# Kernel tuning notes

Measured on AMD Instinct MI355X. Metric: run time of the kernel, lower is better.

Reference implementation:

```python
import jax, jax.numpy as jnp
import numpy as np

OBS, HOR, PD, HID, NH, PROTO = 8, 8, 128, 256, 8, 32
B, N = 8, 4096

def _gelu(x):
    return jax.nn.gelu(x, approximate=False)  # torch nn.GELU default is exact erf

def setup_inputs():
    key = jax.random.key(0)
    ks = iter(jax.random.split(key, 40))
    nrm = lambda shape, s=0.02: jax.random.normal(next(ks), shape, dtype=jnp.float32) * s
    return {
        'obs_points': jax.random.normal(next(ks), (B, N, OBS, 2), dtype=jnp.float32),
        'obs_vis': jax.random.randint(next(ks), (B, N, OBS), 0, 2).astype(bool),
        'rel_xy': jax.random.normal(next(ks), (B, N, 2), dtype=jnp.float32),
        'anchor_obs': jax.random.normal(next(ks), (B, OBS, 2), dtype=jnp.float32),
        'anchor_obs_vel': jax.random.normal(next(ks), (B, OBS, 2), dtype=jnp.float32),
        'semantic_feat': jax.random.normal(next(ks), (B, N, 10), dtype=jnp.float32),
        'ln_w': jnp.ones((OBS * 7,), jnp.float32),
        'ln_b': jnp.zeros((OBS * 7,), jnp.float32),
        'enc_w1': nrm((OBS * 7, PD)), 'enc_b1': jnp.zeros((PD,), jnp.float32),
        'enc_w2': nrm((PD, PD)), 'enc_b2': jnp.zeros((PD,), jnp.float32),
        'time_embed': nrm((HOR, HID)),
        'anchor_w': nrm((OBS * 4, HID)), 'anchor_b': jnp.zeros((HID,), jnp.float32),
        'query_w': nrm((PD, HID)), 'query_b': jnp.zeros((HID,), jnp.float32),
        'in_proj_w': nrm((HID, 3 * HID)), 'in_proj_b': jnp.zeros((3 * HID,), jnp.float32),
        'out_proj_w': nrm((HID, HID)), 'out_proj_b': jnp.zeros((HID,), jnp.float32),
        'ah_w': nrm((HID, 2)), 'ah_b': jnp.zeros((2,), jnp.float32),
        'rh_w1': nrm((HID + PD + 2, HID)), 'rh_b1': jnp.zeros((HID,), jnp.float32),
        'rh_w2': nrm((HID, 2)), 'rh_b2': jnp.zeros((2,), jnp.float32),
        'vh_w1': nrm((HID + PD, HID // 2)), 'vh_b1': jnp.zeros((HID // 2,), jnp.float32),
        'vh_w2': nrm((HID // 2, 1)), 'vh_b2': jnp.zeros((1,), jnp.float32),
        'sh_w': nrm((HID, PROTO)), 'sh_b': jnp.zeros((PROTO,), jnp.float32),
    }

def reference(obs_points, obs_vis, rel_xy, anchor_obs, anchor_obs_vel, semantic_feat,
              ln_w, ln_b, enc_w1, enc_b1, enc_w2, enc_b2, time_embed,
              anchor_w, anchor_b, query_w, query_b, in_proj_w, in_proj_b,
              out_proj_w, out_proj_b, ah_w, ah_b, rh_w1, rh_b1, rh_w2, rh_b2,
              vh_w1, vh_b1, vh_w2, vh_b2, sh_w, sh_b):
    del semantic_feat  # unused, matches original
    Bc, Nc, T, _ = obs_points.shape
    # ---- PointTraceEncoder ----
    vel = jnp.concatenate([jnp.zeros_like(obs_points[:, :, :1]),
                           obs_points[:, :, 1:] - obs_points[:, :, :-1]], axis=2)
    rel = jnp.broadcast_to(rel_xy[:, :, None, :], (Bc, Nc, T, 2))
    feat = jnp.concatenate([obs_points, vel, obs_vis.astype(jnp.float32)[..., None], rel],
                           axis=-1).reshape(Bc, Nc, T * 7)
    mu = feat.mean(-1, keepdims=True)
    var = ((feat - mu) ** 2).mean(-1, keepdims=True)
    x = (feat - mu) / jnp.sqrt(var + 1e-5) * ln_w + ln_b
    point_tokens = _gelu(_gelu(x @ enc_w1 + enc_b1) @ enc_w2 + enc_b2)  # [B,N,PD]
    # ---- queries / memory ----
    anchor_feat = jnp.concatenate([anchor_obs, anchor_obs_vel], -1).reshape(Bc, -1)
    tq = time_embed[None] + (anchor_feat @ anchor_w + anchor_b)[:, None]  # [B,HOR,HID]
    mem = point_tokens @ query_w + query_b  # [B,N,HID]
    # ---- multi-head cross attention ----
    D = tq.shape[-1]; dh = D // NH
    q = tq @ in_proj_w[:, :D] + in_proj_b[:D]
    k = mem @ in_proj_w[:, D:2 * D] + in_proj_b[D:2 * D]
    v = mem @ in_proj_w[:, 2 * D:] + in_proj_b[2 * D:]
    qh = q.reshape(Bc, -1, NH, dh).transpose(0, 2, 1, 3)
    kh = k.reshape(Bc, -1, NH, dh).transpose(0, 2, 1, 3)
    vh = v.reshape(Bc, -1, NH, dh).transpose(0, 2, 1, 3)
    attn = jax.nn.softmax(jnp.einsum('bhqd,bhkd->bhqk', qh, kh) / jnp.sqrt(jnp.float32(dh)), axis=-1)
    o = jnp.einsum('bhqk,bhkd->bhqd', attn, vh).transpose(0, 2, 1, 3).reshape(Bc, -1, D)
    future = o @ out_proj_w + out_proj_b  # [B,HOR,HID]
    # ---- heads ----
    last_anchor = anchor_obs[:, -1]
    anchor_delta = 0.1 * jnp.tanh(future @ ah_w + ah_b)
    anchor_pred = last_anchor[:, None] + jnp.cumsum(anchor_delta, axis=1)  # [B,HOR,2]
    Hq = future.shape[1]
    ft_e = jnp.broadcast_to(future[:, :, None, :], (Bc, Hq, Nc, D))
    pt_e = jnp.broadcast_to(point_tokens[:, None], (Bc, Hq, Nc, point_tokens.shape[-1]))
    rel_e = jnp.broadcast_to(rel_xy[:, None], (Bc, Hq, Nc, 2))
    per_point = jnp.concatenate([ft_e, pt_e, rel_e], axis=-1)  # [B,HOR,N,HID+PD+2]
    residual = 0.1 * jnp.tanh(_gelu(per_point @ rh_w1 + rh_b1) @ rh_w2 + rh_b2)
    pred_points = anchor_pred[:, :, None, :] + residual
    vis_logits = (_gelu(per_point[..., :-2] @ vh_w1 + vh_b1) @ vh_w2 + vh_b2)[..., 0]
    sem_logits = future @ sh_w + sh_b
    return (anchor_pred,
            pred_points.transpose(0, 2, 1, 3),   # [B,N,HOR,2]
            vis_logits.transpose(0, 2, 1),       # [B,N,HOR]
            sem_logits)                           # [B,HOR,PROTO]
```

## Files before the change

### kernel.cpp

```cpp
#include <hip/hip_runtime.h>
#include <math.h>

#define BB 8
#define NN 4096
#define TT 8
#define HORQ 8
#define PD 128
#define HID 256
#define NHD 8
#define DH 32
#define FE 56
#define NC2 16
#define CH2 256

typedef __attribute__((ext_vector_type(8))) short short8;
typedef __attribute__((ext_vector_type(4))) float floatx4;
typedef unsigned short ushort_t;

__device__ __forceinline__ float gelu_fast(float x) {
    float x2 = x * x;
    float y2 = x * fmaf(0.0713551f, x2, 1.5957691f);
    float e = __expf(y2);
    return x - x * __builtin_amdgcn_rcpf(1.f + e);
}

__device__ __forceinline__ float tanh_fast(float x) {
    float e = __expf(2.f * x);
    return 1.f - 2.f * __builtin_amdgcn_rcpf(1.f + e);
}

__device__ __forceinline__ ushort_t f2b(float x) {
    union { float f; unsigned u; } c; c.f = x;
    unsigned r = c.u + 0x7fffu + ((c.u >> 16) & 1u);
    return (ushort_t)(r >> 16);
}
__device__ __forceinline__ float b2f(unsigned hi) {
    union { unsigned u; float f; } c; c.u = hi;
    return c.f;
}

__global__ __launch_bounds__(256) void k_fuse(
    const float* __restrict__ qw, const float* __restrict__ qb,
    const float* __restrict__ ipw, const float* __restrict__ ipb,
    float* __restrict__ Wk, float* __restrict__ Wv,
    float* __restrict__ bk, float* __restrict__ bv)
{
    int j = threadIdx.x;
    int blk = blockIdx.x;
    if (blk < PD) {
        float sk = 0.f, sv = 0.f;
        for (int l = 0; l < HID; l++) {
            float w = qw[blk * HID + l];
            sk += w * ipw[l * 768 + 256 + j];
            sv += w * ipw[l * 768 + 512 + j];
        }
        Wk[blk * HID + j] = sk;
        Wv[blk * HID + j] = sv;
    } else {
        float sk = ipb[256 + j], sv = ipb[512 + j];
        for (int l = 0; l < HID; l++) {
            float w = qb[l];
            sk += w * ipw[l * 768 + 256 + j];
            sv += w * ipw[l * 768 + 512 + j];
        }
        bk[j] = sk;
        bv[j] = sv;
    }
}

__global__ __launch_bounds__(256) void k_prep(
    const float* __restrict__ Wk, const float* __restrict__ Wv,
    const float* __restrict__ rw1, const float* __restrict__ vw1,
    const float* __restrict__ w1, const float* __restrict__ w2,
    const float* __restrict__ aobs, const float* __restrict__ avel,
    const float* __restrict__ te, const float* __restrict__ aw, const float* __restrict__ ab,
    const float* __restrict__ ipw, const float* __restrict__ ipb,
    short* __restrict__ Wfrag, short* __restrict__ w1frag, short* __restrict__ w2frag,
    float* __restrict__ qb_)
{
    __shared__ float af[32];
    __shared__ float tqs[HID];
    int tid = threadIdx.x;
    int blk = blockIdx.x;
    int ks = tid >> 6, lane = tid & 63;
    int quad = lane >> 4, c16 = lane & 15;
    if (blk < 56) {
        int nt = blk;
        int n = nt * 16 + c16;
        for (int j = 0; j < 8; j++) {
            int k = ks * 32 + quad * 8 + j;
            float v;
            if (n < 256)      v = Wk[k * HID + n];
            else if (n < 512) v = Wv[k * HID + (n - 256)];
            else if (n < 768) v = rw1[(256 + k) * HID + (n - 512)];
            else              v = vw1[(256 + k) * PD + (n - 768)];
            Wfrag[((nt * 4 + ks) * 64 + lane) * 8 + j] = (short)f2b(v);
        }
    } else if (blk < 64) {
        if (ks < 2) {
            int nt = blk - 56;
            int n = nt * 16 + c16;
            for (int j = 0; j < 8; j++) {
                int k = ks * 32 + quad * 8 + j;
                float v = (k < FE) ? w1[k * PD + n] : 0.f;
                w1frag[((nt * 2 + ks) * 64 + lane) * 8 + j] = (short)f2b(v);
            }
        }
    } else if (blk < 72) {
        int nt = blk - 64;
        int n = nt * 16 + c16;
        for (int j = 0; j < 8; j++) {
            int k = ks * 32 + quad * 8 + j;
            w2frag[((nt * 4 + ks) * 64 + lane) * 8 + j] = (short)f2b(w2[k * PD + n]);
        }
    } else {
        int bh = blk - 72;
        int b = bh >> 3, h = bh & 7;
        if (tid < 32) {
            int t = tid >> 2, m = tid & 3;
            af[tid] = (m < 2) ? aobs[(b * TT + t) * 2 + m] : avel[(b * TT + t) * 2 + (m - 2)];
        }
        __syncthreads();
        float s = te[h * HID + tid] + ab[tid];
        for (int i = 0; i < 32; i++) s += af[i] * aw[i * HID + tid];
        tqs[tid] = s;
        __syncthreads();
        float qv = ipb[tid];
        for (int i = 0; i < HID; i++) qv += tqs[i] * ipw[i * 768 + tid];
        qb_[(size_t)bh * HID + tid] = qv;
    }
}

#define U1_OFF 0
#define XNB_OFF 17408
#define PTB_OFF 26624
#define RXY_OFF 44032
#define MU_OFF 44544
#define RS_OFF 44800
#define SMEM_BYTES 45056

__global__ __launch_bounds__(256) void k_main(
    const float* __restrict__ obs, const int* __restrict__ vis,
    const float* __restrict__ rel,
    const float* __restrict__ lnw, const float* __restrict__ lnb,
    const float* __restrict__ b1, const float* __restrict__ b2,
    const short* __restrict__ Wfrag, const short* __restrict__ w1frag,
    const short* __restrict__ w2frag,
    const float* __restrict__ bk, const float* __restrict__ bv,
    const float* __restrict__ rw1,
    ushort_t* __restrict__ kb, ushort_t* __restrict__ vb,
    ushort_t* __restrict__ P1, ushort_t* __restrict__ P2)
{
    __shared__ __align__(16) char smem[SMEM_BYTES];
    float* xnf = (float*)(smem + U1_OFF);
    short* h1b = (short*)(smem + U1_OFF);
    short* xnb = (short*)(smem + XNB_OFF);
    short* ptb = (short*)(smem + PTB_OFF);
    float* rxyS = (float*)(smem + RXY_OFF);
    float* muS = (float*)(smem + MU_OFF);
    float* rsS = (float*)(smem + RS_OFF);

    int tid = threadIdx.x;
    int w = tid >> 6, lane = tid & 63;
    int quad = lane >> 4, c16 = lane & 15;
    int bn0 = blockIdx.x * 64;

    for (int idx = tid; idx < 64 * FE; idx += 256) {
        int p = idx / FE, e = idx - p * FE;
        int t = e / 7, c = e - t * 7;
        int bn = bn0 + p;
        float v;
        if (c < 2)       v = obs[(bn * TT + t) * 2 + c];
        else if (c < 4)  v = (t == 0) ? 0.f : (obs[(bn * TT + t) * 2 + (c - 2)] - obs[(bn * TT + t - 1) * 2 + (c - 2)]);
        else if (c == 4) v = (float)vis[bn * TT + t];
        else             v = rel[bn * 2 + (c - 5)];
        xnf[p * 57 + e] = v;
    }
    if (tid < 128) rxyS[tid] = rel[bn0 * 2 + tid];
    __syncthreads();

    if (tid < 64) {
        float s = 0.f, ss = 0.f;
        for (int e = 0; e < FE; e++) { float v = xnf[tid * 57 + e]; s += v; ss += v * v; }
        float mu = s * (1.f / FE);
        float var = ss * (1.f / FE) - mu * mu;
        muS[tid] = mu;
        rsS[tid] = rsqrtf(var + 1e-5f);
    }
    __syncthreads();

    for (int idx = tid; idx < 64 * 64; idx += 256) {
        int p = idx >> 6, e = idx & 63;
        float v = 0.f;
        if (e < FE) v = (xnf[p * 57 + e] - muS[p]) * rsS[p] * lnw[e] + lnb[e];
        xnb[p * 72 + e] = (short)f2b(v);
    }
    __syncthreads();

    {
        short8 af1[4][2];
        #pragma unroll
        for (int mt = 0; mt < 4; mt++)
            #pragma unroll
            for (int ks = 0; ks < 2; ks++)
                af1[mt][ks] = *(const short8*)(xnb + (mt * 16 + c16) * 72 + ks * 32 + quad * 8);
        #pragma unroll
        for (int ntl = 0; ntl < 2; ntl++) {
            int nt = w * 2 + ntl;
            short8 bf1[2];
            #pragma unroll
            for (int ks = 0; ks < 2; ks++)
                bf1[ks] = *(const short8*)(w1frag + ((nt * 2 + ks) * 64 + lane) * 8);
            int col = nt * 16 + c16;
            float bb = b1[col];
            #pragma unroll
            for (int mt = 0; mt < 4; mt++) {
                floatx4 acc = {0.f, 0.f, 0.f, 0.f};
                acc = __builtin_amdgcn_mfma_f32_16x16x32_bf16(af1[mt][0], bf1[0], acc, 0, 0, 0);
                acc = __builtin_amdgcn_mfma_f32_16x16x32_bf16(af1[mt][1], bf1[1], acc, 0, 0, 0);
                #pragma unroll
                for (int r = 0; r < 4; r++) {
                    int row = mt * 16 + quad * 4 + r;
                    h1b[row * 136 + col] = (short)f2b(gelu_fast(acc[r] + bb));
                }
            }
        }
    }
    __syncthreads();

    {
        short8 af2[4][4];
        #pragma unroll
        for (int mt = 0; mt < 4; mt++)
            #pragma unroll
            for (int ks = 0; ks < 4; ks++)
                af2[mt][ks] = *(const short8*)(h1b + (mt * 16 + c16) * 136 + ks * 32 + quad * 8);
        #pragma unroll
        for (int ntl = 0; ntl < 2; ntl++) {
            int nt = w * 2 + ntl;
            short8 bf2[4];
            #pragma unroll
            for (int ks = 0; ks < 4; ks++)
                bf2[ks] = *(const short8*)(w2frag + ((nt * 4 + ks) * 64 + lane) * 8);
            int col = nt * 16 + c16;
            float bb = b2[col];
            #pragma unroll
            for (int mt = 0; mt < 4; mt++) {
                floatx4 acc = {0.f, 0.f, 0.f, 0.f};
                #pragma unroll
                for (int ks = 0; ks < 4; ks++)
                    acc = __builtin_amdgcn_mfma_f32_16x16x32_bf16(af2[mt][ks], bf2[ks], acc, 0, 0, 0);
                #pragma unroll
                for (int r = 0; r < 4; r++) {
                    int row = mt * 16 + quad * 4 + r;
                    ptb[row * 136 + col] = (short)f2b(gelu_fast(acc[r] + bb));
                }
            }
        }
    }
    __syncthreads();

    {
        short8 af[4][4];
        #pragma unroll
        for (int mt = 0; mt < 4; mt++)
            #pragma unroll
            for (int ks = 0; ks < 4; ks++)
                af[mt][ks] = *(const short8*)(ptb + (mt * 16 + c16) * 136 + ks * 32 + quad * 8);
        for (int i = 0; i < 14; i++) {
            int nt = w + i * 4;
            short8 bf[4];
            #pragma unroll
            for (int ks = 0; ks < 4; ks++)
                bf[ks] = *(const short8*)(Wfrag + ((nt * 4 + ks) * 64 + lane) * 8);
            floatx4 acc[4];
            #pragma unroll
            for (int mt = 0; mt < 4; mt++) {
                acc[mt] = (floatx4){0.f, 0.f, 0.f, 0.f};
                #pragma unroll
                for (int ks = 0; ks < 4; ks++)
                    acc[mt] = __builtin_amdgcn_mfma_f32_16x16x32_bf16(af[mt][ks], bf[ks], acc[mt], 0, 0, 0);
            }
            int n = nt * 16 + c16;
            if (nt < 16) {
                float bb = bk[n];
                #pragma unroll
                for (int mt = 0; mt < 4; mt++)
                    #pragma unroll
                    for (int r = 0; r < 4; r++) {
                        int row = mt * 16 + quad * 4 + r;
                        kb[(size_t)(bn0 + row) * HID + n] = f2b(acc[mt][r] + bb);
                    }
            } else if (nt < 32) {
                int j = n - 256;
                float bb = bv[j];
                #pragma unroll
                for (int mt = 0; mt < 4; mt++)
                    #pragma unroll
                    for (int r = 0; r < 4; r++) {
                        int row = mt * 16 + quad * 4 + r;
                        vb[(size_t)(bn0 + row) * HID + j] = f2b(acc[mt][r] + bb);
                    }
            } else if (nt < 48) {
                int j = n - 512;
                float wr0 = rw1[384 * HID + j], wr1 = rw1[385 * HID + j];
                #pragma unroll
                for (int mt = 0; mt < 4; mt++)
                    #pragma unroll
                    for (int r = 0; r < 4; r++) {
                        int row = mt * 16 + quad * 4 + r;
                        P1[(size_t)(bn0 + row) * HID + j] =
                            f2b(acc[mt][r] + rxyS[row * 2] * wr0 + rxyS[row * 2 + 1] * wr1);
                    }
            } else {
                int j = n - 768;
                #pragma unroll
                for (int mt = 0; mt < 4; mt++)
                    #pragma unroll
                    for (int r = 0; r < 4; r++) {
                        int row = mt * 16 + quad * 4 + r;
                        P2[(size_t)(bn0 + row) * PD + j] = f2b(acc[mt][r]);
                    }
            }
        }
    }
}

__global__ __launch_bounds__(256) void k_att(
    const float* __restrict__ qbuf, const ushort_t* __restrict__ kb, const ushort_t* __restrict__ vbuf,
    float* __restrict__ pm, float* __restrict__ pl, float* __restrict__ po)
{
    __shared__ float qs[8][DH];
    __shared__ float sc[8][CH2];
    __shared__ float pos[8][8][DH];
    int tid = threadIdx.x;
    int bidx = blockIdx.x;
    int c = bidx & (NC2 - 1);
    int head = (bidx >> 4) & 7;
    int b = bidx >> 7;
    qs[tid >> 5][tid & 31] = qbuf[(size_t)(b * HORQ + (tid >> 5)) * HID + head * DH + (tid & 31)];
    __syncthreads();
    const float scale = 0.17677669529663688110f;
    {
        int nn = tid;
        int n = c * CH2 + nn;
        const ushort_t* kp = kb + (size_t)(b * NN + n) * HID + head * DH;
        float kr[DH];
        #pragma unroll
        for (int u = 0; u < 4; u++) {
            uint4 q = *reinterpret_cast<const uint4*>(kp + u * 8);
            unsigned wd[4] = {q.x, q.y, q.z, q.w};
            #pragma unroll
            for (int t2 = 0; t2 < 4; t2++) {
                kr[u * 8 + 2 * t2]     = b2f(wd[t2] << 16);
                kr[u * 8 + 2 * t2 + 1] = b2f(wd[t2] & 0xffff0000u);
            }
        }
        #pragma unroll
        for (int qq = 0; qq < 8; qq++) {
            float s = 0.f;
            #pragma unroll
            for (int d = 0; d < DH; d++) s += qs[qq][d] * kr[d];
            sc[qq][nn] = s * scale;
        }
    }
    __syncthreads();
    int qq = tid >> 5, r = tid & 31;
    float mx = -1e30f;
    #pragma unroll
    for (int nn = r; nn < CH2; nn += 32) mx = fmaxf(mx, sc[qq][nn]);
    #pragma unroll
    for (int m = 16; m; m >>= 1) mx = fmaxf(mx, __shfl_xor(mx, m, 32));
    float sum = 0.f;
    #pragma unroll
    for (int nn = r; nn < CH2; nn += 32) { float e = __expf(sc[qq][nn] - mx); sc[qq][nn] = e; sum += e; }
    #pragma unroll
    for (int m = 16; m; m >>= 1) sum += __shfl_xor(sum, m, 32);
    if (r == 0) { pm[bidx * 8 + qq] = mx; pl[bidx * 8 + qq] = sum; }
    __syncthreads();
    {
        int g = tid >> 5, d = tid & 31;
        float oacc[8];
        #pragma unroll
        for (int q2 = 0; q2 < 8; q2++) oacc[q2] = 0.f;
        const ushort_t* vp = vbuf + ((size_t)(b * NN + c * CH2 + g * 32)) * HID + head * DH + d;
        for (int i = 0; i < 32; i++) {
            float v = b2f(((unsigned)vp[(size_t)i * HID]) << 16);
            int nn = g * 32 + i;
            #pragma unroll
            for (int q2 = 0; q2 < 8; q2++) oacc[q2] += sc[q2][nn] * v;
        }
        #pragma unroll
        for (int q2 = 0; q2 < 8; q2++) pos[g][q2][d] = oacc[q2];
    }
    __syncthreads();
    {
        int q2 = tid >> 5, d = tid & 31;
        float o = 0.f;
        #pragma unroll
        for (int gg = 0; gg < 8; gg++) o += pos[gg][q2][d];
        po[(size_t)(bidx * 8 + q2) * DH + d] = o;
    }
}

__global__ __launch_bounds__(256) void k_attfut(
    const float* __restrict__ pm, const float* __restrict__ pl, const float* __restrict__ po,
    const float* __restrict__ opw, const float* __restrict__ opb,
    const float* __restrict__ rw1, const float* __restrict__ rb1,
    const float* __restrict__ vw1, const float* __restrict__ vb1,
    const float* __restrict__ shw, const float* __restrict__ shb,
    const float* __restrict__ ahw, const float* __restrict__ ahb,
    float* __restrict__ F1, float* __restrict__ F2, float* __restrict__ dl, float* __restrict__ sem)
{
    __shared__ float orow[HID], fut[HID];
    int tid = threadIdx.x;
    int b = blockIdx.x >> 3, qq = blockIdx.x & 7;
    {
        int head = tid >> 5, d = tid & 31;
        int base = b * 1024 + head * 128 + qq;
        float M = -1e30f;
        #pragma unroll
        for (int c = 0; c < NC2; c++) M = fmaxf(M, pm[base + c * 8]);
        float L = 0.f, o = 0.f;
        #pragma unroll
        for (int c = 0; c < NC2; c++) {
            float wgt = __expf(pm[base + c * 8] - M);
            L += wgt * pl[base + c * 8];
            o += wgt * po[(size_t)(base + c * 8) * DH + d];
        }
        orow[head * DH + d] = o / L;
    }
    __syncthreads();
    float s = opb[tid];
    for (int i = 0; i < HID; i++) s += orow[i] * opw[i * HID + tid];
    fut[tid] = s;
    __syncthreads();
    int bh = b * HORQ + qq;
    float f1 = rb1[tid];
    for (int i = 0; i < HID; i++) f1 += fut[i] * rw1[i * HID + tid];
    F1[(size_t)bh * HID + tid] = f1;
    if (tid < PD) {
        float f2 = vb1[tid];
        for (int i = 0; i < HID; i++) f2 += fut[i] * vw1[i * PD + tid];
        F2[(size_t)bh * PD + tid] = f2;
    }
    if (tid < 32) {
        float s3 = shb[tid];
        for (int i = 0; i < HID; i++) s3 += fut[i] * shw[i * 32 + tid];
        sem[bh * 32 + tid] = s3;
    }
    if (tid < 2) {
        float a = ahb[tid];
        for (int i = 0; i < HID; i++) a += fut[i] * ahw[i * 2 + tid];
        dl[bh * 2 + tid] = 0.1f * tanhf(a);
    }
}

__global__ void k_cum(const float* __restrict__ aobs, const float* __restrict__ dl, float* __restrict__ out0)
{
    int tid = threadIdx.x;
    if (tid < 16) {
        int b = tid >> 1, c = tid & 1;
        float acc = aobs[(b * TT + 7) * 2 + c];
        for (int h = 0; h < HORQ; h++) {
            acc += dl[(b * HORQ + h) * 2 + c];
            out0[(b * HORQ + h) * 2 + c] = acc;
        }
    }
}

__global__ __launch_bounds__(256) void k_fin(
    const float* __restrict__ F1, const float* __restrict__ F2,
    const ushort_t* __restrict__ P1, const ushort_t* __restrict__ P2,
    const float* __restrict__ rw2, const float* __restrict__ rb2,
    const float* __restrict__ vw2, const float* __restrict__ vb2,
    const float* __restrict__ ap,
    float* __restrict__ out1, float* __restrict__ out2)
{
    int tid = threadIdx.x;
    int sub = tid >> 5;
    int l = tid & 31;
    int bn = blockIdx.x * 8 + sub;
    int b = bn >> 12;

    uint4 q1 = *(const uint4*)(P1 + (size_t)bn * HID + l * 8);
    float p1f[8];
    {
        unsigned wd[4] = {q1.x, q1.y, q1.z, q1.w};
        #pragma unroll
        for (int u = 0; u < 4; u++) {
            p1f[2 * u]     = b2f(wd[u] << 16);
            p1f[2 * u + 1] = b2f(wd[u] & 0xffff0000u);
        }
    }
    float w0[8], w1[8];
    {
        const float4* rwp = (const float4*)(rw2 + l * 16);
        #pragma unroll
        for (int u = 0; u < 4; u++) {
            float4 r = rwp[u];
            w0[2 * u] = r.x; w1[2 * u] = r.y;
            w0[2 * u + 1] = r.z; w1[2 * u + 1] = r.w;
        }
    }
    float p2f[4];
    {
        uint2 q2 = *(const uint2*)(P2 + (size_t)bn * PD + l * 4);
        p2f[0] = b2f(q2.x << 16); p2f[1] = b2f(q2.x & 0xffff0000u);
        p2f[2] = b2f(q2.y << 16); p2f[3] = b2f(q2.y & 0xffff0000u);
    }
    float4 wvv = *(const float4*)(vw2 + l * 4);
    float wv[4] = {wvv.x, wvv.y, wvv.z, wvv.w};

    float rb20 = rb2[0], rb21 = rb2[1], vb20 = vb2[0];
    for (int h = 0; h < HORQ; h++) {
        const float* f1p = F1 + (size_t)(b * HORQ + h) * HID + l * 8;
        float4 fa = *(const float4*)f1p;
        float4 fb = *(const float4*)(f1p + 4);
        float f1r[8] = {fa.x, fa.y, fa.z, fa.w, fb.x, fb.y, fb.z, fb.w};
        float4 f2v = *(const float4*)(F2 + (size_t)(b * HORQ + h) * PD + l * 4);
        float f2r[4] = {f2v.x, f2v.y, f2v.z, f2v.w};
        float s0 = 0.f, s1 = 0.f, sv = 0.f;
        #pragma unroll
        for (int u = 0; u < 8; u++) {
            float g = gelu_fast(f1r[u] + p1f[u]);
            s0 += g * w0[u];
            s1 += g * w1[u];
        }
        #pragma unroll
        for (int u = 0; u < 4; u++) {
            float g = gelu_fast(f2r[u] + p2f[u]);
            sv += g * wv[u];
        }
        #pragma unroll
        for (int m = 16; m; m >>= 1) {
            s0 += __shfl_xor(s0, m, 32);
            s1 += __shfl_xor(s1, m, 32);
            sv += __shfl_xor(sv, m, 32);
        }
        if (l == 0) {
            float rx = 0.1f * tanh_fast(s0 + rb20);
            float ry = 0.1f * tanh_fast(s1 + rb21);
            int bh = b * HORQ + h;
            out1[((size_t)bn * HORQ + h) * 2 + 0] = ap[bh * 2 + 0] + rx;
            out1[((size_t)bn * HORQ + h) * 2 + 1] = ap[bh * 2 + 1] + ry;
            out2[(size_t)bn * HORQ + h] = sv + vb20;
        }
    }
}

extern "C" void kernel_launch(void* const* d_in, const int* in_sizes, int n_in,
                              void* d_out, int out_size, void* d_ws, size_t ws_size,
                              hipStream_t stream)
{
    const float* obs  = (const float*)d_in[0];
    const int*   vis  = (const int*)d_in[1];
    const float* rel  = (const float*)d_in[2];
    const float* aobs = (const float*)d_in[3];
    const float* avel = (const float*)d_in[4];
    const float* lnw = (const float*)d_in[6];
    const float* lnb = (const float*)d_in[7];
    const float* ew1 = (const float*)d_in[8];
    const float* eb1 = (const float*)d_in[9];
    const float* ew2 = (const float*)d_in[10];
    const float* eb2 = (const float*)d_in[11];
    const float* te  = (const float*)d_in[12];
    const float* aw  = (const float*)d_in[13];
    const float* ab  = (const float*)d_in[14];
    const float* qw  = (const float*)d_in[15];
    const float* qbias = (const float*)d_in[16];
    const float* ipw = (const float*)d_in[17];
    const float* ipb = (const float*)d_in[18];
    const float* opw = (const float*)d_in[19];
    const float* opb = (const float*)d_in[20];
    const float* ahw = (const float*)d_in[21];
    const float* ahb = (const float*)d_in[22];
    const float* rw1 = (const float*)d_in[23];
    const float* rb1 = (const float*)d_in[24];
    const float* rw2 = (const float*)d_in[25];
    const float* rb2 = (const float*)d_in[26];
    const float* vw1 = (const float*)d_in[27];
    const float* vb1 = (const float*)d_in[28];
    const float* vw2 = (const float*)d_in[29];
    const float* vb2 = (const float*)d_in[30];
    const float* shw = (const float*)d_in[31];
    const float* shb = (const float*)d_in[32];

    float* W = (float*)d_ws;
    size_t o = 0;
    float* Wk  = W + o; o += (size_t)PD * HID;
    float* Wv  = W + o; o += (size_t)PD * HID;
    float* bk  = W + o; o += HID;
    float* bv  = W + o; o += HID;
    float* qb_ = W + o; o += (size_t)BB * HORQ * HID;
    float* F1  = W + o; o += (size_t)BB * HORQ * HID;
    float* F2  = W + o; o += (size_t)BB * HORQ * PD;
    float* dl  = W + o; o += (size_t)BB * HORQ * 2;
    float* pm  = W + o; o += (size_t)BB * NHD * NC2 * 8;
    float* pl  = W + o; o += (size_t)BB * NHD * NC2 * 8;
    float* po  = W + o; o += (size_t)BB * NHD * NC2 * 8 * DH;
    ushort_t* kb   = (ushort_t*)(W + o); o += (size_t)BB * NN * HID / 2;
    ushort_t* vbuf = (ushort_t*)(W + o); o += (size_t)BB * NN * HID / 2;
    ushort_t* P1   = (ushort_t*)(W + o); o += (size_t)BB * NN * HID / 2;
    ushort_t* P2   = (ushort_t*)(W + o); o += (size_t)BB * NN * PD / 2;
    short* Sf = (short*)(W + o);
    short* Wfrag  = Sf;
    short* w1frag = Sf + 114688;
    short* w2frag = Sf + 114688 + 8192;

    float* out0 = (float*)d_out;
    float* out1 = out0 + BB * HORQ * 2;
    float* out2 = out1 + (size_t)BB * NN * HORQ * 2;
    float* out3 = out2 + (size_t)BB * NN * HORQ;

    k_fuse<<<PD + 1, 256, 0, stream>>>(qw, qbias, ipw, ipb, Wk, Wv, bk, bv);
    k_prep<<<72 + 64, 256, 0, stream>>>(Wk, Wv, rw1, vw1, ew1, ew2,
                                        aobs, avel, te, aw, ab, ipw, ipb,
                                        Wfrag, w1frag, w2frag, qb_);
    k_main<<<BB * NN / 64, 256, 0, stream>>>(obs, vis, rel, lnw, lnb, eb1, eb2,
                                             Wfrag, w1frag, w2frag, bk, bv, rw1,
                                             kb, vbuf, P1, P2);
    k_att<<<BB * NHD * NC2, 256, 0, stream>>>(qb_, kb, vbuf, pm, pl, po);
    k_attfut<<<BB * HORQ, 256, 0, stream>>>(pm, pl, po, opw, opb, rw1, rb1, vw1, vb1,
                                            shw, shb, ahw, ahb, F1, F2, dl, out3);
    k_cum<<<1, 64, 0, stream>>>(aobs, dl, out0);
    k_fin<<<BB * NN / 8, 256, 0, stream>>>(F1, F2, P1, P2, rw2, rb2, vw2, vb2,
                                           out0, out1, out2);
}
```

Before: 273.8 us.

## Add ILP accumulators, parallelize reductions, restructure attention scoring and packed FMAs

Splits the serial dot-product loops in the weight-fusion, prep and head kernels into four independent accumulators to break FMA dependency chains. Parallelizes the layernorm statistics across four threads per row and the semantic and anchor heads across lanes with shuffle reductions. Attention scoring now keeps q in registers and has each thread score eight keys, dropping the shared q buffer and a barrier. The final kernel uses packed float2 FMAs and partial unrolling. Accumulation order changes slightly, so float results may differ in the last bits.

```diff
diff --git a/kernel.cpp b/kernel.cpp
--- a/kernel.cpp
+++ b/kernel.cpp
@@ -15,6 +15,7 @@
 
 typedef __attribute__((ext_vector_type(8))) short short8;
 typedef __attribute__((ext_vector_type(4))) float floatx4;
+typedef __attribute__((ext_vector_type(2))) float floatx2;
 typedef unsigned short ushort_t;
 
 __device__ __forceinline__ float gelu_fast(float x) {
@@ -47,24 +48,27 @@
 {
     int j = threadIdx.x;
     int blk = blockIdx.x;
+    const float* src = (blk < PD) ? (qw + blk * HID) : qb;
+    float sk0 = 0.f, sk1 = 0.f, sk2 = 0.f, sk3 = 0.f;
+    float sv0 = 0.f, sv1 = 0.f, sv2 = 0.f, sv3 = 0.f;
+    for (int l = 0; l < HID; l += 4) {
+        float w0 = src[l], w1 = src[l + 1], w2 = src[l + 2], w3 = src[l + 3];
+        sk0 += w0 * ipw[l * 768 + 256 + j];
+        sk1 += w1 * ipw[(l + 1) * 768 + 256 + j];
+        sk2 += w2 * ipw[(l + 2) * 768 + 256 + j];
+        sk3 += w3 * ipw[(l + 3) * 768 + 256 + j];
+        sv0 += w0 * ipw[l * 768 + 512 + j];
+        sv1 += w1 * ipw[(l + 1) * 768 + 512 + j];
+        sv2 += w2 * ipw[(l + 2) * 768 + 512 + j];
+        sv3 += w3 * ipw[(l + 3) * 768 + 512 + j];
+    }
+    float sk = sk0 + sk1 + sk2 + sk3, sv = sv0 + sv1 + sv2 + sv3;
     if (blk < PD) {
-        float sk = 0.f, sv = 0.f;
-        for (int l = 0; l < HID; l++) {
-            float w = qw[blk * HID + l];
-            sk += w * ipw[l * 768 + 256 + j];
-            sv += w * ipw[l * 768 + 512 + j];
-        }
         Wk[blk * HID + j] = sk;
         Wv[blk * HID + j] = sv;
     } else {
-        float sk = ipb[256 + j], sv = ipb[512 + j];
-        for (int l = 0; l < HID; l++) {
-            float w = qb[l];
-            sk += w * ipw[l * 768 + 256 + j];
-            sv += w * ipw[l * 768 + 512 + j];
-        }
-        bk[j] = sk;
-        bv[j] = sv;
+        bk[j] = sk + ipb[256 + j];
+        bv[j] = sv + ipb[512 + j];
     }
 }
 
@@ -125,9 +129,14 @@
         for (int i = 0; i < 32; i++) s += af[i] * aw[i * HID + tid];
         tqs[tid] = s;
         __syncthreads();
-        float qv = ipb[tid];
-        for (int i = 0; i < HID; i++) qv += tqs[i] * ipw[i * 768 + tid];
-        qb_[(size_t)bh * HID + tid] = qv;
+        float q0 = ipb[tid], q1 = 0.f, q2 = 0.f, q3 = 0.f;
+        for (int i = 0; i < HID; i += 4) {
+            q0 += tqs[i] * ipw[i * 768 + tid];
+            q1 += tqs[i + 1] * ipw[(i + 1) * 768 + tid];
+            q2 += tqs[i + 2] * ipw[(i + 2) * 768 + tid];
+            q3 += tqs[i + 3] * ipw[(i + 3) * 768 + tid];
+        }
+        qb_[(size_t)bh * HID + tid] = q0 + q1 + q2 + q3;
     }
 }
 
@@ -165,27 +174,37 @@
     int quad = lane >> 4, c16 = lane & 15;
     int bn0 = blockIdx.x * 64;
 
-    for (int idx = tid; idx < 64 * FE; idx += 256) {
-        int p = idx / FE, e = idx - p * FE;
-        int t = e / 7, c = e - t * 7;
+    #pragma unroll
+    for (int u = 0; u < 2; u++) {
+        int pair = tid + u * 256;
+        int p = pair >> 3, t = pair & 7;
         int bn = bn0 + p;
-        float v;
-        if (c < 2)       v = obs[(bn * TT + t) * 2 + c];
-        else if (c < 4)  v = (t == 0) ? 0.f : (obs[(bn * TT + t) * 2 + (c - 2)] - obs[(bn * TT + t - 1) * 2 + (c - 2)]);
-        else if (c == 4) v = (float)vis[bn * TT + t];
-        else             v = rel[bn * 2 + (c - 5)];
-        xnf[p * 57 + e] = v;
+        float2 oc = *(const float2*)(obs + (bn * TT + t) * 2);
+        int tp = t ? (t - 1) : 0;
+        float2 op = *(const float2*)(obs + (bn * TT + tp) * 2);
+        float dx = t ? (oc.x - op.x) : 0.f;
+        float dy = t ? (oc.y - op.y) : 0.f;
+        float vv = (float)vis[bn * TT + t];
+        float2 rl = *(const float2*)(rel + bn * 2);
+        float* xp = xnf + p * 57 + t * 7;
+        xp[0] = oc.x; xp[1] = oc.y; xp[2] = dx; xp[3] = dy;
+        xp[4] = vv; xp[5] = rl.x; xp[6] = rl.y;
     }
     if (tid < 128) rxyS[tid] = rel[bn0 * 2 + tid];
     __syncthreads();
 
-    if (tid < 64) {
+    {
+        int p = tid >> 2, r = tid & 3;
         float s = 0.f, ss = 0.f;
-        for (int e = 0; e < FE; e++) { float v = xnf[tid * 57 + e]; s += v; ss += v * v; }
-        float mu = s * (1.f / FE);
-        float var = ss * (1.f / FE) - mu * mu;
-        muS[tid] = mu;
-        rsS[tid] = rsqrtf(var + 1e-5f);
+        for (int e = r; e < FE; e += 4) { float v = xnf[p * 57 + e]; s += v; ss += v * v; }
+        s += __shfl_xor(s, 1); ss += __shfl_xor(ss, 1);
+        s += __shfl_xor(s, 2); ss += __shfl_xor(ss, 2);
+        if (r == 0) {
+            float mu = s * (1.f / FE);
+            float var = ss * (1.f / FE) - mu * mu;
+            muS[p] = mu;
+            rsS[p] = rsqrtf(var + 1e-5f);
+        }
     }
     __syncthreads();
 
@@ -330,7 +349,6 @@
     const float* __restrict__ qbuf, const ushort_t* __restrict__ kb, const ushort_t* __restrict__ vbuf,
     float* __restrict__ pm, float* __restrict__ pl, float* __restrict__ po)
 {
-    __shared__ float qs[8][DH];
     __shared__ float sc[8][CH2];
     __shared__ float pos[8][8][DH];
     int tid = threadIdx.x;
@@ -338,29 +356,31 @@
     int c = bidx & (NC2 - 1);
     int head = (bidx >> 4) & 7;
     int b = bidx >> 7;
-    qs[tid >> 5][tid & 31] = qbuf[(size_t)(b * HORQ + (tid >> 5)) * HID + head * DH + (tid & 31)];
-    __syncthreads();
     const float scale = 0.17677669529663688110f;
     {
-        int nn = tid;
-        int n = c * CH2 + nn;
-        const ushort_t* kp = kb + (size_t)(b * NN + n) * HID + head * DH;
-        float kr[DH];
-        #pragma unroll
-        for (int u = 0; u < 4; u++) {
-            uint4 q = *reinterpret_cast<const uint4*>(kp + u * 8);
-            unsigned wd[4] = {q.x, q.y, q.z, q.w};
-            #pragma unroll
-            for (int t2 = 0; t2 < 4; t2++) {
-                kr[u * 8 + 2 * t2]     = b2f(wd[t2] << 16);
-                kr[u * 8 + 2 * t2 + 1] = b2f(wd[t2] & 0xffff0000u);
+        int qq = tid >> 5, ln = tid & 31;
+        float qr[DH];
+        const float* qp = qbuf + (size_t)(b * HORQ + qq) * HID + head * DH;
+        #pragma unroll
+        for (int u = 0; u < 8; u++) {
+            float4 f = *(const float4*)(qp + u * 4);
+            qr[u * 4] = f.x; qr[u * 4 + 1] = f.y; qr[u * 4 + 2] = f.z; qr[u * 4 + 3] = f.w;
+        }
+        #pragma unroll
+        for (int i = 0; i < 8; i++) {
+            int nn = ln + 32 * i;
+            const ushort_t* kp = kb + (size_t)(b * NN + c * CH2 + nn) * HID + head * DH;
+            float s = 0.f;
+            #pragma unroll
+            for (int u = 0; u < 4; u++) {
+                uint4 q = *(const uint4*)(kp + u * 8);
+                unsigned wd[4] = {q.x, q.y, q.z, q.w};
+                #pragma unroll
+                for (int t2 = 0; t2 < 4; t2++) {
+                    s += qr[u * 8 + 2 * t2]     * b2f(wd[t2] << 16);
+                    s += qr[u * 8 + 2 * t2 + 1] * b2f(wd[t2] & 0xffff0000u);
+                }
             }
-        }
-        #pragma unroll
-        for (int qq = 0; qq < 8; qq++) {
-            float s = 0.f;
-            #pragma unroll
-            for (int d = 0; d < DH; d++) s += qs[qq][d] * kr[d];
             sc[qq][nn] = s * scale;
         }
     }
@@ -431,28 +451,55 @@
         orow[head * DH + d] = o / L;
     }
     __syncthreads();
-    float s = opb[tid];
-    for (int i = 0; i < HID; i++) s += orow[i] * opw[i * HID + tid];
-    fut[tid] = s;
+    {
+        float a0 = opb[tid], a1 = 0.f, a2 = 0.f, a3 = 0.f;
+        for (int i = 0; i < HID; i += 4) {
+            a0 += orow[i] * opw[i * HID + tid];
+            a1 += orow[i + 1] * opw[(i + 1) * HID + tid];
+            a2 += orow[i + 2] * opw[(i + 2) * HID + tid];
+            a3 += orow[i + 3] * opw[(i + 3) * HID + tid];
+        }
+        fut[tid] = a0 + a1 + a2 + a3;
+    }
     __syncthreads();
     int bh = b * HORQ + qq;
-    float f1 = rb1[tid];
-    for (int i = 0; i < HID; i++) f1 += fut[i] * rw1[i * HID + tid];
-    F1[(size_t)bh * HID + tid] = f1;
+    {
+        float a0 = rb1[tid], a1 = 0.f, a2 = 0.f, a3 = 0.f;
+        for (int i = 0; i < HID; i += 4) {
+            a0 += fut[i] * rw1[i * HID + tid];
+            a1 += fut[i + 1] * rw1[(i + 1) * HID + tid];
+            a2 += fut[i + 2] * rw1[(i + 2) * HID + tid];
+            a3 += fut[i + 3] * rw1[(i + 3) * HID + tid];
+        }
+        F1[(size_t)bh * HID + tid] = a0 + a1 + a2 + a3;
+    }
     if (tid < PD) {
-        float f2 = vb1[tid];
-        for (int i = 0; i < HID; i++) f2 += fut[i] * vw1[i * PD + tid];
-        F2[(size_t)bh * PD + tid] = f2;
-    }
-    if (tid < 32) {
-        float s3 = shb[tid];
-        for (int i = 0; i < HID; i++) s3 += fut[i] * shw[i * 32 + tid];
-        sem[bh * 32 + tid] = s3;
-    }
-    if (tid < 2) {
-        float a = ahb[tid];
-        for (int i = 0; i < HID; i++) a += fut[i] * ahw[i * 2 + tid];
-        dl[bh * 2 + tid] = 0.1f * tanhf(a);
+        float a0 = vb1[tid], a1 = 0.f, a2 = 0.f, a3 = 0.f;
+        for (int i = 0; i < HID; i += 4) {
+            a0 += fut[i] * vw1[i * PD + tid];
+            a1 += fut[i + 1] * vw1[(i + 1) * PD + tid];
+            a2 += fut[i + 2] * vw1[(i + 2) * PD + tid];
+            a3 += fut[i + 3] * vw1[(i + 3) * PD + tid];
+        }
+        F2[(size_t)bh * PD + tid] = a0 + a1 + a2 + a3;
+    }
+    {
+        int j = tid >> 3, part = tid & 7;
+        float s3 = 0.f;
+        for (int i = part * 32; i < part * 32 + 32; i++) s3 += fut[i] * shw[i * 32 + j];
+        s3 += __shfl_xor(s3, 1);
+        s3 += __shfl_xor(s3, 2);
+        s3 += __shfl_xor(s3, 4);
+        if (part == 0) sem[bh * 32 + j] = s3 + shb[j];
+    }
+    if (tid < 128) {
+        int j = tid >> 6, part = tid & 63;
+        float a = 0.f;
+        #pragma unroll
+        for (int u = 0; u < 4; u++) { int i = part * 4 + u; a += fut[i] * ahw[i * 2 + j]; }
+        #pragma unroll
+        for (int m = 32; m; m >>= 1) a += __shfl_xor(a, m);
+        if (part == 0) dl[bh * 2 + j] = 0.1f * tanhf(a + ahb[j]);
     }
 }
 
@@ -493,14 +540,14 @@
             p1f[2 * u + 1] = b2f(wd[u] & 0xffff0000u);
         }
     }
-    float w0[8], w1[8];
+    floatx2 w01[8];
     {
         const float4* rwp = (const float4*)(rw2 + l * 16);
         #pragma unroll
         for (int u = 0; u < 4; u++) {
             float4 r = rwp[u];
-            w0[2 * u] = r.x; w1[2 * u] = r.y;
-            w0[2 * u + 1] = r.z; w1[2 * u + 1] = r.w;
+            w01[2 * u] = (floatx2){r.x, r.y};
+            w01[2 * u + 1] = (floatx2){r.z, r.w};
         }
     }
     float p2f[4];
@@ -513,6 +560,7 @@
     float wv[4] = {wvv.x, wvv.y, wvv.z, wvv.w};
 
     float rb20 = rb2[0], rb21 = rb2[1], vb20 = vb2[0];
+    #pragma unroll 2
     for (int h = 0; h < HORQ; h++) {
         const float* f1p = F1 + (size_t)(b * HORQ + h) * HID + l * 8;
         float4 fa = *(const float4*)f1p;
@@ -520,18 +568,19 @@
         float f1r[8] = {fa.x, fa.y, fa.z, fa.w, fb.x, fb.y, fb.z, fb.w};
         float4 f2v = *(const float4*)(F2 + (size_t)(b * HORQ + h) * PD + l * 4);
         float f2r[4] = {f2v.x, f2v.y, f2v.z, f2v.w};
-        float s0 = 0.f, s1 = 0.f, sv = 0.f;
+        floatx2 s01 = {0.f, 0.f};
+        float sv = 0.f;
         #pragma unroll
         for (int u = 0; u < 8; u++) {
             float g = gelu_fast(f1r[u] + p1f[u]);
-            s0 += g * w0[u];
-            s1 += g * w1[u];
+            s01 += (floatx2){g, g} * w01[u];
         }
         #pragma unroll
         for (int u = 0; u < 4; u++) {
             float g = gelu_fast(f2r[u] + p2f[u]);
             sv += g * wv[u];
         }
+        float s0 = s01.x, s1 = s01.y;
         #pragma unroll
         for (int m = 16; m; m >>= 1) {
             s0 += __shfl_xor(s0, m, 32);
```

Result: faster. 260.5 us (-4.8%).
